# Kernel tuning notes

Measured on AMD Instinct MI355X. Metric: run time of the kernel, lower is better.

The kernel has to match this reference:

```python
import jax, jax.numpy as jnp
import numpy as np

KERNEL_SIZE = 9  # spatial kernel extent used only for output cropping


def setup_inputs() -> dict:
    key = jax.random.key(0)
    k1, k2, k3, k4 = jax.random.split(key, 4)
    B, Cin, Cout, H, W = 32, 64, 128, 128, 128
    Wf = W // 2 + 1  # rfft bins on last dim (W even, no pad branch)
    return {
        "signal": jax.random.normal(k1, (B, Cin, H, W), dtype=jnp.float32),
        "weight_real": jax.random.normal(k2, (Cout, Cin, H, Wf), dtype=jnp.float32),
        "weight_imag": jax.random.normal(k3, (Cout, Cin, H, Wf), dtype=jnp.float32),
        "bias": jax.random.normal(k4, (Cout,), dtype=jnp.float32),
    }


def reference(signal, weight_real, weight_imag, bias):
    # FFT conv with a frequency-domain complex kernel (groups=1, padding=0,
    # stride=1). Matches torch fft_conv: rfftn -> complex matmul over channels
    # per frequency bin -> irfftn -> crop -> bias add.
    B, Cin, H, W = signal.shape
    sig_fr = jnp.fft.rfftn(signal, axes=(2, 3))            # [B, Cin, H, W//2+1] c64
    kernel = (weight_real + 1j * weight_imag).astype(jnp.complex64)
    # complex_matmul with groups=1: contract Cin per (h,w) frequency bin
    out_fr = jnp.einsum('bihw,oihw->bohw', sig_fr, kernel)  # [B, Cout, H, W//2+1]
    out = jnp.fft.irfftn(out_fr, axes=(2, 3))               # [B, Cout, H, W] real
    Ho = H - KERNEL_SIZE + 1
    Wo = W - KERNEL_SIZE + 1
    out = out[:, :, :Ho, :Wo]
    out = out + bias[None, :, None, None]
    return out
```

## Files before the change

### kernel.cpp

```cpp
#include <hip/hip_runtime.h>
#include <math.h>

#define DI __device__ __forceinline__

constexpr int Hh   = 128;
constexpr int Ww   = 128;
constexpr int WF   = 65;
constexpr int NBIN = Hh * WF;
constexpr int NB   = 32;
constexpr int CIN  = 64;
constexpr int COUT = 128;
constexpr int HO   = 120;
constexpr int WO   = 120;

typedef __bf16 bf16x8 __attribute__((ext_vector_type(8)));
typedef float  f32x16 __attribute__((ext_vector_type(16)));

DI unsigned int bfbits(float x) {
  unsigned int u = __float_as_uint(x);
  return (u + 0x7FFFu + ((u >> 16) & 1u)) >> 16;
}
DI unsigned int packbf(float re, float im) { return bfbits(re) | (bfbits(im) << 16); }
DI float2 unpackbf(unsigned int v) {
  return make_float2(__uint_as_float(v << 16), __uint_as_float(v & 0xFFFF0000u));
}

DI f32x16 MFMA32(uint4 a, uint4 b, f32x16 c) {
  return __builtin_amdgcn_mfma_f32_32x32x16_bf16(
      __builtin_bit_cast(bf16x8, a), __builtin_bit_cast(bf16x8, b), c, 0, 0, 0);
}
DI unsigned int rotneg(unsigned int x) { return ((x << 16) | (x >> 16)) ^ 0x80000000u; }
DI uint4 derive(uint4 s) {
  uint4 r; r.x = rotneg(s.x); r.y = rotneg(s.y); r.z = rotneg(s.z); r.w = rotneg(s.w);
  return r;
}

DI void wsync() {
  asm volatile("s_waitcnt lgkmcnt(0)" ::: "memory");
  __builtin_amdgcn_sched_barrier(0);
}

DI float2* fft128x2(float2* s, float2* d, const float2* tw, int lane, int inv) {
  wsync();
#pragma unroll
  for (int st = 0; st < 7; ++st) {
    const int m  = 1 << st;
    const int tj = lane & ~(m - 1);
    float2 a0 = s[lane],       a1 = s[lane + 64];
    float2 b0 = s[lane + 128], b1 = s[lane + 192];
    float2 w  = tw[tj];
    const float wy = inv ? -w.y : w.y;
    const int di = lane + tj;
    {
      float sx = a0.x + a1.x, sy = a0.y + a1.y;
      float dx = a0.x - a1.x, dy = a0.y - a1.y;
      d[di]     = make_float2(sx, sy);
      d[di + m] = make_float2(w.x * dx - wy * dy, w.x * dy + wy * dx);
    }
    {
      float sx = b0.x + b1.x, sy = b0.y + b1.y;
      float dx = b0.x - b1.x, dy = b0.y - b1.y;
      d[di + 128]     = make_float2(sx, sy);
      d[di + 128 + m] = make_float2(w.x * dx - wy * dy, w.x * dy + wy * dx);
    }
    wsync();
    float2* t_ = s; s = d; d = t_;
  }
  return s;
}

__global__ __launch_bounds__(256) void fwd_fft(const float* __restrict__ sig,
                                               unsigned int* __restrict__ sf) {
  __shared__ unsigned int sImg[NBIN];
  __shared__ float2 bufA[4][256];
  __shared__ float2 bufB[4][256];
  __shared__ float2 tw[64];

  const int t = threadIdx.x, grp = t >> 6, lane = t & 63;
  const size_t img = blockIdx.x;
  const float* src = sig + img * (size_t)(Hh * Ww);
  unsigned int* dst = sf + img * (size_t)NBIN;

  if (t < 64) {
    float s_, c_;
    sincosf(-(float)M_PI * (float)t / 64.f, &s_, &c_);
    tw[t] = make_float2(c_, s_);
  }
  __syncthreads();

  for (int batch = 0; batch < 8; ++batch) {
#pragma unroll
    for (int f = 0; f < 2; ++f) {
      const int jp = batch * 8 + grp * 2 + f;
      const float* r0 = src + (size_t)(2 * jp) * Ww;
      bufA[grp][f * 128 + lane]      = make_float2(r0[lane],      r0[Ww + lane]);
      bufA[grp][f * 128 + 64 + lane] = make_float2(r0[lane + 64], r0[Ww + lane + 64]);
    }
    float2* Z = fft128x2(bufA[grp], bufB[grp], tw, lane, 0);
#pragma unroll
    for (int f = 0; f < 2; ++f) {
      const int jp = batch * 8 + grp * 2 + f;
      float2 Zk = Z[f * 128 + lane];
      float2 Zm = Z[f * 128 + ((128 - lane) & 127)];
      sImg[(2 * jp) * WF + lane]     = packbf(0.5f * (Zk.x + Zm.x), 0.5f * (Zk.y - Zm.y));
      sImg[(2 * jp + 1) * WF + lane] = packbf(0.5f * (Zk.y + Zm.y), 0.5f * (Zm.x - Zk.x));
      if (lane == 0) {
        float2 Z64 = Z[f * 128 + 64];
        sImg[(2 * jp) * WF + 64]     = packbf(Z64.x, 0.f);
        sImg[(2 * jp + 1) * WF + 64] = packbf(Z64.y, 0.f);
      }
    }
  }
  __syncthreads();

  for (int batch = 0; batch < 9; ++batch) {
#pragma unroll
    for (int f = 0; f < 2; ++f) {
      const int w  = batch * 8 + grp * 2 + f;
      const int wc = (w < WF) ? w : (WF - 1);
      bufA[grp][f * 128 + lane]      = unpackbf(sImg[lane * WF + wc]);
      bufA[grp][f * 128 + 64 + lane] = unpackbf(sImg[(lane + 64) * WF + wc]);
    }
    float2* R = fft128x2(bufA[grp], bufB[grp], tw, lane, 0);
#pragma unroll
    for (int f = 0; f < 2; ++f) {
      const int w = batch * 8 + grp * 2 + f;
      if (w < WF) {
        float2 a = R[f * 128 + lane], b = R[f * 128 + 64 + lane];
        sImg[lane * WF + w]        = packbf(a.x, a.y);
        sImg[(lane + 64) * WF + w] = packbf(b.x, b.y);
      }
    }
  }
  __syncthreads();

  const uint4* s4 = (const uint4*)sImg;
  uint4* d4 = (uint4*)dst;
  for (int idx = t; idx < NBIN / 4; idx += 256) d4[idx] = s4[idx];
}

constexpr int PT    = 16;
constexpr int PLANE = 260;

__global__ __launch_bounds__(512, 4) void spec_mm(const unsigned int* __restrict__ sf,
                                                  const float* __restrict__ wr,
                                                  const float* __restrict__ wi,
                                                  unsigned int* __restrict__ of) {
  __shared__ unsigned int wbuf[PT * PLANE];
  __shared__ unsigned int sbuf[PT * PLANE];

  const int t = threadIdx.x;
  const int bid = blockIdx.x;
  const int swz = (bid & 7) * 260 + (bid >> 3);
  const int o0 = (swz & 3) * 32;
  const int p0 = (swz >> 2) * PT;

  const int po = t & 3;
  const int ii = (t >> 2) & 7;
  const int rl = (t >> 5) & 15;

  const float* wrp0 = wr + ((size_t)(o0 + rl) * CIN + ii) * NBIN + p0 + po * 4;
  const float* wip0 = wi + ((size_t)(o0 + rl) * CIN + ii) * NBIN + p0 + po * 4;
  const unsigned int* sfp0 = sf + ((size_t)rl * CIN + ii) * NBIN + p0 + po * 4;
  const size_t rowAdv = (size_t)16 * CIN * NBIN;

  auto slotOf = [](int row, int i) {
    return ((((row * 2) + (i >> 2)) ^ ((row >> 2) & 7)) << 2) + (i & 3);
  };
  const int slotLo = slotOf(rl, ii);
  const int slotHi = slotOf(rl + 16, ii);

  const int l = t & 63, wv = t >> 6;
  const int lr = l & 31, lq = l >> 5;
  const int moff = ((((lr * 2) + lq) ^ ((lr >> 2) & 7)) << 2);
  const int pA = 2 * wv, pB = 2 * wv + 1;

  f32x16 aR0 = {}, aI0 = {}, aR1 = {}, aI1 = {};

  float4 w0r, w1r, w0i, w1i; uint4 s0v, s1v;
  {
    w0r = *(const float4*)(wrp0);          w1r = *(const float4*)(wrp0 + rowAdv);
    w0i = *(const float4*)(wip0);          w1i = *(const float4*)(wip0 + rowAdv);
    s0v = *(const uint4*)(sfp0);           s1v = *(const uint4*)(sfp0 + rowAdv);
  }

  for (int kq = 0; kq < 8; ++kq) {
    const float* a0 = (const float*)&w0r;  const float* a1 = (const float*)&w1r;
    const float* b0 = (const float*)&w0i;  const float* b1 = (const float*)&w1i;
    const unsigned int* u0 = (const unsigned int*)&s0v;
    const unsigned int* u1 = (const unsigned int*)&s1v;
#pragma unroll
    for (int j = 0; j < 4; ++j) {
      const int pp = (po * 4 + j) * PLANE;
      wbuf[pp + slotLo] = packbf(a0[j], -b0[j]);
      wbuf[pp + slotHi] = packbf(a1[j], -b1[j]);
      sbuf[pp + slotLo] = u0[j];
      sbuf[pp + slotHi] = u1[j];
    }
    if (kq < 7) {
      const size_t adv = (size_t)(kq + 1) * 8 * NBIN;
      w0r = *(const float4*)(wrp0 + adv);          w1r = *(const float4*)(wrp0 + adv + rowAdv);
      w0i = *(const float4*)(wip0 + adv);          w1i = *(const float4*)(wip0 + adv + rowAdv);
      s0v = *(const uint4*)(sfp0 + adv);           s1v = *(const uint4*)(sfp0 + adv + rowAdv);
    }
    __syncthreads();

    {
      const uint4 a  = *(const uint4*)&wbuf[pA * PLANE + moff];
      const uint4 s  = *(const uint4*)&sbuf[pA * PLANE + moff];
      aR0 = MFMA32(a, s, aR0);
      aI0 = MFMA32(a, derive(s), aI0);
    }
    {
      const uint4 a  = *(const uint4*)&wbuf[pB * PLANE + moff];
      const uint4 s  = *(const uint4*)&sbuf[pB * PLANE + moff];
      aR1 = MFMA32(a, s, aR1);
      aI1 = MFMA32(a, derive(s), aI1);
    }
    __syncthreads();
  }

  const int b = lr;
#pragma unroll
  for (int r = 0; r < 16; ++r) {
    const int o = o0 + (r & 3) + 8 * (r >> 2) + 4 * lq;
    uint2 v;
    v.x = packbf(aR0[r], aI0[r]);
    v.y = packbf(aR1[r], aI1[r]);
    *(uint2*)(of + ((size_t)b * COUT + o) * NBIN + p0 + 2 * wv) = v;
  }
}

__global__ __launch_bounds__(256) void inv_fft(const unsigned int* __restrict__ of,
                                               const float* __restrict__ bias,
                                               float* __restrict__ out) {
  __shared__ unsigned int sImg[NBIN];
  __shared__ float2 bufA[4][256];
  __shared__ float2 bufB[4][256];
  __shared__ float2 tw[64];

  const int t = threadIdx.x, grp = t >> 6, lane = t & 63;
  const size_t img = blockIdx.x;
  const unsigned int* src = of + img * (size_t)NBIN;
  float* dst = out + img * (size_t)(HO * WO);
  const float bo = bias[img & (COUT - 1)];

  if (t < 64) {
    float s_, c_;
    sincosf(-(float)M_PI * (float)t / 64.f, &s_, &c_);
    tw[t] = make_float2(c_, s_);
  }

  const uint4* s4 = (const uint4*)src;
  uint4* d4 = (uint4*)sImg;
  for (int idx = t; idx < NBIN / 4; idx += 256) d4[idx] = s4[idx];
  __syncthreads();

  for (int batch = 0; batch < 9; ++batch) {
#pragma unroll
    for (int f = 0; f < 2; ++f) {
      const int w  = batch * 8 + grp * 2 + f;
      const int wc = (w < WF) ? w : (WF - 1);
      bufA[grp][f * 128 + lane]      = unpackbf(sImg[lane * WF + wc]);
      bufA[grp][f * 128 + 64 + lane] = unpackbf(sImg[(lane + 64) * WF + wc]);
    }
    float2* R = fft128x2(bufA[grp], bufB[grp], tw, lane, 1);
#pragma unroll
    for (int f = 0; f < 2; ++f) {
      const int w = batch * 8 + grp * 2 + f;
      if (w < WF) {
        float2 a = R[f * 128 + lane], b = R[f * 128 + 64 + lane];
        sImg[lane * WF + w]        = packbf(a.x, a.y);
        sImg[(lane + 64) * WF + w] = packbf(b.x, b.y);
      }
    }
  }
  __syncthreads();

  const float scale = 1.f / 16384.f;
  for (int batch = 0; batch < 8; ++batch) {
#pragma unroll
    for (int f = 0; f < 2; ++f) {
      const int jp = batch * 8 + grp * 2 + f;
      const int jc = (jp < 60) ? jp : 59;
      const unsigned int* X0p = &sImg[(size_t)(2 * jc) * WF];
      const unsigned int* X1p = X0p + WF;
      float2 za, zb;
      if (lane == 0) {
        za = make_float2(unpackbf(X0p[0]).x,  unpackbf(X1p[0]).x);
        zb = make_float2(unpackbf(X0p[64]).x, unpackbf(X1p[64]).x);
      } else {
        float2 x0 = unpackbf(X0p[lane]), x1 = unpackbf(X1p[lane]);
        za = make_float2(x0.x - x1.y, x0.y + x1.x);
        const int mI = 64 - lane;
        float2 y0 = unpackbf(X0p[mI]), y1 = unpackbf(X1p[mI]);
        zb = make_float2(y0.x + y1.y, y1.x - y0.y);
      }
      bufA[grp][f * 128 + lane]      = za;
      bufA[grp][f * 128 + 64 + lane] = zb;
    }
    float2* R = fft128x2(bufA[grp], bufB[grp], tw, lane, 1);
#pragma unroll
    for (int f = 0; f < 2; ++f) {
      const int jp = batch * 8 + grp * 2 + f;
      if (jp < 60) {
        float2 v0 = R[f * 128 + lane];
        dst[(size_t)(2 * jp) * WO + lane]     = v0.x * scale + bo;
        dst[(size_t)(2 * jp + 1) * WO + lane] = v0.y * scale + bo;
        if (lane < WO - 64) {
          float2 v1 = R[f * 128 + 64 + lane];
          dst[(size_t)(2 * jp) * WO + lane + 64]     = v1.x * scale + bo;
          dst[(size_t)(2 * jp + 1) * WO + lane + 64] = v1.y * scale + bo;
        }
      }
    }
  }
}

extern "C" void kernel_launch(void* const* d_in, const int* in_sizes, int n_in,
                              void* d_out, int out_size, void* d_ws, size_t ws_size,
                              hipStream_t stream) {
  const float* signal = (const float*)d_in[0];
  const float* wr     = (const float*)d_in[1];
  const float* wi     = (const float*)d_in[2];
  const float* bias   = (const float*)d_in[3];
  float* out = (float*)d_out;

  unsigned int* sig_fr = (unsigned int*)d_out;
  unsigned int* out_fr = (unsigned int*)d_ws;
  (void)in_sizes; (void)n_in; (void)out_size; (void)ws_size;

  fwd_fft<<<NB * CIN, 256, 0, stream>>>(signal, sig_fr);
  spec_mm<<<2080, 512, 0, stream>>>(sig_fr, wr, wi, out_fr);
  inv_fft<<<NB * COUT, 256, 0, stream>>>(out_fr, bias, out);
}
```

Before: 546.7 us.

## Use wave-shuffle register FFTs and double-buffer spec_mm global prefetch

```diff
diff --git a/kernel.cpp b/kernel.cpp
--- a/kernel.cpp
+++ b/kernel.cpp
@@ -40,95 +40,121 @@
   __builtin_amdgcn_sched_barrier(0);
 }
 
-DI float2* fft128x2(float2* s, float2* d, const float2* tw, int lane, int inv) {
-  wsync();
-#pragma unroll
-  for (int st = 0; st < 7; ++st) {
-    const int m  = 1 << st;
-    const int tj = lane & ~(m - 1);
-    float2 a0 = s[lane],       a1 = s[lane + 64];
-    float2 b0 = s[lane + 128], b1 = s[lane + 192];
-    float2 w  = tw[tj];
-    const float wy = inv ? -w.y : w.y;
-    const int di = lane + tj;
-    {
-      float sx = a0.x + a1.x, sy = a0.y + a1.y;
-      float dx = a0.x - a1.x, dy = a0.y - a1.y;
-      d[di]     = make_float2(sx, sy);
-      d[di + m] = make_float2(w.x * dx - wy * dy, w.x * dy + wy * dx);
-    }
-    {
-      float sx = b0.x + b1.x, sy = b0.y + b1.y;
-      float dx = b0.x - b1.x, dy = b0.y - b1.y;
-      d[di + 128]     = make_float2(sx, sy);
-      d[di + 128 + m] = make_float2(w.x * dx - wy * dy, w.x * dy + wy * dx);
-    }
-    wsync();
-    float2* t_ = s; s = d; d = t_;
-  }
-  return s;
+DI int bitrev6(int l) {
+  return ((l & 1) << 5) | ((l & 2) << 3) | ((l & 4) << 1) |
+         ((l & 8) >> 1) | ((l & 16) >> 3) | ((l & 32) >> 5);
+}
+DI float2 cmul(float2 a, float2 b) {
+  return make_float2(a.x * b.x - a.y * b.y, a.x * b.y + a.y * b.x);
+}
+DI float2 sxor(float2 v, int m) {
+  return make_float2(__shfl_xor(v.x, m), __shfl_xor(v.y, m));
+}
+DI void stg(float2& v, int h, float2 tw, int l) {
+  float2 p = sxor(v, h);
+  float2 s = make_float2(v.x + p.x, v.y + p.y);
+  float2 d = make_float2(p.x - v.x, p.y - v.y);
+  float2 m = cmul(d, tw);
+  v = (l & h) ? m : s;
+}
+DI void stg1(float2& v, int l) {
+  float2 p = sxor(v, 1);
+  v = (l & 1) ? make_float2(p.x - v.x, p.y - v.y)
+              : make_float2(v.x + p.x, v.y + p.y);
+}
+DI void twinit(float2* tw, int l) {
+  float s_, c_;
+  sincosf(-(float)M_PI * (float)l / 64.f, &s_, &c_);
+  tw[0] = make_float2(c_, s_);
+#pragma unroll
+  for (int i = 0; i < 5; ++i) {
+    const int h = 32 >> i;
+    sincosf(-(float)M_PI * (float)(l & (h - 1)) / (float)h, &s_, &c_);
+    tw[1 + i] = make_float2(c_, s_);
+  }
+}
+DI void sfft128x2(float2& a0, float2& b0, float2& a1, float2& b1,
+                  const float2* tw, int l) {
+  {
+    float2 s = make_float2(a0.x + b0.x, a0.y + b0.y);
+    float2 d = make_float2(a0.x - b0.x, a0.y - b0.y);
+    a0 = s; b0 = cmul(d, tw[0]);
+  }
+  {
+    float2 s = make_float2(a1.x + b1.x, a1.y + b1.y);
+    float2 d = make_float2(a1.x - b1.x, a1.y - b1.y);
+    a1 = s; b1 = cmul(d, tw[0]);
+  }
+#pragma unroll
+  for (int i = 0; i < 5; ++i) {
+    const int h = 32 >> i;
+    stg(a0, h, tw[1 + i], l); stg(a1, h, tw[1 + i], l);
+    stg(b0, h, tw[1 + i], l); stg(b1, h, tw[1 + i], l);
+  }
+  stg1(a0, l); stg1(a1, l); stg1(b0, l); stg1(b1, l);
 }
 
 __global__ __launch_bounds__(256) void fwd_fft(const float* __restrict__ sig,
                                                unsigned int* __restrict__ sf) {
   __shared__ unsigned int sImg[NBIN];
-  __shared__ float2 bufA[4][256];
-  __shared__ float2 bufB[4][256];
-  __shared__ float2 tw[64];
-
-  const int t = threadIdx.x, grp = t >> 6, lane = t & 63;
+  __shared__ __align__(16) float2 rowbuf[4][2][128];
+
+  const int t = threadIdx.x, grp = t >> 6, l = t & 63;
   const size_t img = blockIdx.x;
   const float* src = sig + img * (size_t)(Hh * Ww);
   unsigned int* dst = sf + img * (size_t)NBIN;
 
-  if (t < 64) {
-    float s_, c_;
-    sincosf(-(float)M_PI * (float)t / 64.f, &s_, &c_);
-    tw[t] = make_float2(c_, s_);
-  }
-  __syncthreads();
+  float2 tw[6]; twinit(tw, l);
+  const int br = bitrev6(l);
 
   for (int batch = 0; batch < 8; ++batch) {
+    float2 a[2], b[2];
 #pragma unroll
     for (int f = 0; f < 2; ++f) {
       const int jp = batch * 8 + grp * 2 + f;
       const float* r0 = src + (size_t)(2 * jp) * Ww;
-      bufA[grp][f * 128 + lane]      = make_float2(r0[lane],      r0[Ww + lane]);
-      bufA[grp][f * 128 + 64 + lane] = make_float2(r0[lane + 64], r0[Ww + lane + 64]);
-    }
-    float2* Z = fft128x2(bufA[grp], bufB[grp], tw, lane, 0);
+      a[f] = make_float2(r0[l],      r0[Ww + l]);
+      b[f] = make_float2(r0[64 + l], r0[Ww + 64 + l]);
+    }
+    sfft128x2(a[0], b[0], a[1], b[1], tw, l);
+#pragma unroll
+    for (int f = 0; f < 2; ++f) {
+      *(float4*)&rowbuf[grp][f][2 * br] =
+          make_float4(a[f].x, a[f].y, b[f].x, b[f].y);
+    }
+    wsync();
 #pragma unroll
     for (int f = 0; f < 2; ++f) {
       const int jp = batch * 8 + grp * 2 + f;
-      float2 Zk = Z[f * 128 + lane];
-      float2 Zm = Z[f * 128 + ((128 - lane) & 127)];
-      sImg[(2 * jp) * WF + lane]     = packbf(0.5f * (Zk.x + Zm.x), 0.5f * (Zk.y - Zm.y));
-      sImg[(2 * jp + 1) * WF + lane] = packbf(0.5f * (Zk.y + Zm.y), 0.5f * (Zm.x - Zk.x));
-      if (lane == 0) {
-        float2 Z64 = Z[f * 128 + 64];
+      float2 Zk = rowbuf[grp][f][l];
+      float2 Zm = rowbuf[grp][f][(128 - l) & 127];
+      sImg[(2 * jp) * WF + l]     = packbf(0.5f * (Zk.x + Zm.x), 0.5f * (Zk.y - Zm.y));
+      sImg[(2 * jp + 1) * WF + l] = packbf(0.5f * (Zk.y + Zm.y), 0.5f * (Zm.x - Zk.x));
+      if (l == 0) {
+        float2 Z64 = rowbuf[grp][f][64];
         sImg[(2 * jp) * WF + 64]     = packbf(Z64.x, 0.f);
         sImg[(2 * jp + 1) * WF + 64] = packbf(Z64.y, 0.f);
       }
     }
+    wsync();
   }
   __syncthreads();
 
   for (int batch = 0; batch < 9; ++batch) {
-#pragma unroll
-    for (int f = 0; f < 2; ++f) {
-      const int w  = batch * 8 + grp * 2 + f;
+    float2 a[2], b[2]; int wcol[2];
+#pragma unroll
+    for (int f = 0; f < 2; ++f) {
+      const int w = batch * 8 + grp * 2 + f; wcol[f] = w;
       const int wc = (w < WF) ? w : (WF - 1);
-      bufA[grp][f * 128 + lane]      = unpackbf(sImg[lane * WF + wc]);
-      bufA[grp][f * 128 + 64 + lane] = unpackbf(sImg[(lane + 64) * WF + wc]);
-    }
-    float2* R = fft128x2(bufA[grp], bufB[grp], tw, lane, 0);
-#pragma unroll
-    for (int f = 0; f < 2; ++f) {
-      const int w = batch * 8 + grp * 2 + f;
-      if (w < WF) {
-        float2 a = R[f * 128 + lane], b = R[f * 128 + 64 + lane];
-        sImg[lane * WF + w]        = packbf(a.x, a.y);
-        sImg[(lane + 64) * WF + w] = packbf(b.x, b.y);
+      a[f] = unpackbf(sImg[l * WF + wc]);
+      b[f] = unpackbf(sImg[(l + 64) * WF + wc]);
+    }
+    sfft128x2(a[0], b[0], a[1], b[1], tw, l);
+#pragma unroll
+    for (int f = 0; f < 2; ++f) {
+      if (wcol[f] < WF) {
+        sImg[(2 * br) * WF + wcol[f]]     = packbf(a[f].x, a[f].y);
+        sImg[(2 * br + 1) * WF + wcol[f]] = packbf(b[f].x, b[f].y);
       }
     }
   }
@@ -142,7 +168,7 @@
 constexpr int PT    = 16;
 constexpr int PLANE = 260;
 
-__global__ __launch_bounds__(512, 4) void spec_mm(const unsigned int* __restrict__ sf,
+__global__ __launch_bounds__(512, 3) void spec_mm(const unsigned int* __restrict__ sf,
                                                   const float* __restrict__ wr,
                                                   const float* __restrict__ wi,
                                                   unsigned int* __restrict__ of) {
@@ -177,43 +203,50 @@
 
   f32x16 aR0 = {}, aI0 = {}, aR1 = {}, aI1 = {};
 
-  float4 w0r, w1r, w0i, w1i; uint4 s0v, s1v;
-  {
-    w0r = *(const float4*)(wrp0);          w1r = *(const float4*)(wrp0 + rowAdv);
-    w0i = *(const float4*)(wip0);          w1i = *(const float4*)(wip0 + rowAdv);
-    s0v = *(const uint4*)(sfp0);           s1v = *(const uint4*)(sfp0 + rowAdv);
-  }
-
+  float4 w0r[2], w1r[2], w0i[2], w1i[2]; uint4 s0v[2], s1v[2];
+
+#pragma unroll
+  for (int s = 0; s < 2; ++s) {
+    const size_t adv = (size_t)s * 8 * NBIN;
+    w0r[s] = *(const float4*)(wrp0 + adv);  w1r[s] = *(const float4*)(wrp0 + adv + rowAdv);
+    w0i[s] = *(const float4*)(wip0 + adv);  w1i[s] = *(const float4*)(wip0 + adv + rowAdv);
+    s0v[s] = *(const uint4*)(sfp0 + adv);   s1v[s] = *(const uint4*)(sfp0 + adv + rowAdv);
+  }
+
+#pragma unroll
   for (int kq = 0; kq < 8; ++kq) {
-    const float* a0 = (const float*)&w0r;  const float* a1 = (const float*)&w1r;
-    const float* b0 = (const float*)&w0i;  const float* b1 = (const float*)&w1i;
-    const unsigned int* u0 = (const unsigned int*)&s0v;
-    const unsigned int* u1 = (const unsigned int*)&s1v;
-#pragma unroll
-    for (int j = 0; j < 4; ++j) {
-      const int pp = (po * 4 + j) * PLANE;
-      wbuf[pp + slotLo] = packbf(a0[j], -b0[j]);
-      wbuf[pp + slotHi] = packbf(a1[j], -b1[j]);
-      sbuf[pp + slotLo] = u0[j];
-      sbuf[pp + slotHi] = u1[j];
-    }
-    if (kq < 7) {
-      const size_t adv = (size_t)(kq + 1) * 8 * NBIN;
-      w0r = *(const float4*)(wrp0 + adv);          w1r = *(const float4*)(wrp0 + adv + rowAdv);
-      w0i = *(const float4*)(wip0 + adv);          w1i = *(const float4*)(wip0 + adv + rowAdv);
-      s0v = *(const uint4*)(sfp0 + adv);           s1v = *(const uint4*)(sfp0 + adv + rowAdv);
+    const int cs = kq & 1;
+    {
+      const float* a0 = (const float*)&w0r[cs]; const float* a1 = (const float*)&w1r[cs];
+      const float* b0 = (const float*)&w0i[cs]; const float* b1 = (const float*)&w1i[cs];
+      const unsigned int* u0 = (const unsigned int*)&s0v[cs];
+      const unsigned int* u1 = (const unsigned int*)&s1v[cs];
+#pragma unroll
+      for (int j = 0; j < 4; ++j) {
+        const int pp = (po * 4 + j) * PLANE;
+        wbuf[pp + slotLo] = packbf(a0[j], -b0[j]);
+        wbuf[pp + slotHi] = packbf(a1[j], -b1[j]);
+        sbuf[pp + slotLo] = u0[j];
+        sbuf[pp + slotHi] = u1[j];
+      }
+    }
+    if (kq < 6) {
+      const size_t adv = (size_t)(kq + 2) * 8 * NBIN;
+      w0r[cs] = *(const float4*)(wrp0 + adv);  w1r[cs] = *(const float4*)(wrp0 + adv + rowAdv);
+      w0i[cs] = *(const float4*)(wip0 + adv);  w1i[cs] = *(const float4*)(wip0 + adv + rowAdv);
+      s0v[cs] = *(const uint4*)(sfp0 + adv);   s1v[cs] = *(const uint4*)(sfp0 + adv + rowAdv);
     }
     __syncthreads();
 
     {
-      const uint4 a  = *(const uint4*)&wbuf[pA * PLANE + moff];
-      const uint4 s  = *(const uint4*)&sbuf[pA * PLANE + moff];
+      const uint4 a = *(const uint4*)&wbuf[pA * PLANE + moff];
+      const uint4 s = *(const uint4*)&sbuf[pA * PLANE + moff];
       aR0 = MFMA32(a, s, aR0);
       aI0 = MFMA32(a, derive(s), aI0);
     }
     {
-      const uint4 a  = *(const uint4*)&wbuf[pB * PLANE + moff];
-      const uint4 s  = *(const uint4*)&sbuf[pB * PLANE + moff];
+      const uint4 a = *(const uint4*)&wbuf[pB * PLANE + moff];
+      const uint4 s = *(const uint4*)&sbuf[pB * PLANE + moff];
       aR1 = MFMA32(a, s, aR1);
       aI1 = MFMA32(a, derive(s), aI1);
     }
@@ -235,21 +268,15 @@
                                                const float* __restrict__ bias,
                                                float* __restrict__ out) {
   __shared__ unsigned int sImg[NBIN];
-  __shared__ float2 bufA[4][256];
-  __shared__ float2 bufB[4][256];
-  __shared__ float2 tw[64];
-
-  const int t = threadIdx.x, grp = t >> 6, lane = t & 63;
+
+  const int t = threadIdx.x, grp = t >> 6, l = t & 63;
   const size_t img = blockIdx.x;
   const unsigned int* src = of + img * (size_t)NBIN;
   float* dst = out + img * (size_t)(HO * WO);
   const float bo = bias[img & (COUT - 1)];
 
-  if (t < 64) {
-    float s_, c_;
-    sincosf(-(float)M_PI * (float)t / 64.f, &s_, &c_);
-    tw[t] = make_float2(c_, s_);
-  }
+  float2 tw[6]; twinit(tw, l);
+  const int br = bitrev6(l);
 
   const uint4* s4 = (const uint4*)src;
   uint4* d4 = (uint4*)sImg;
@@ -257,61 +284,60 @@
   __syncthreads();
 
   for (int batch = 0; batch < 9; ++batch) {
-#pragma unroll
-    for (int f = 0; f < 2; ++f) {
-      const int w  = batch * 8 + grp * 2 + f;
+    float2 a[2], b[2]; int wcol[2];
+#pragma unroll
+    for (int f = 0; f < 2; ++f) {
+      const int w = batch * 8 + grp * 2 + f; wcol[f] = w;
       const int wc = (w < WF) ? w : (WF - 1);
-      bufA[grp][f * 128 + lane]      = unpackbf(sImg[lane * WF + wc]);
-      bufA[grp][f * 128 + 64 + lane] = unpackbf(sImg[(lane + 64) * WF + wc]);
-    }
-    float2* R = fft128x2(bufA[grp], bufB[grp], tw, lane, 1);
-#pragma unroll
-    for (int f = 0; f < 2; ++f) {
-      const int w = batch * 8 + grp * 2 + f;
-      if (w < WF) {
-        float2 a = R[f * 128 + lane], b = R[f * 128 + 64 + lane];
-        sImg[lane * WF + w]        = packbf(a.x, a.y);
-        sImg[(lane + 64) * WF + w] = packbf(b.x, b.y);
+      float2 za = unpackbf(sImg[l * WF + wc]);
+      float2 zb = unpackbf(sImg[(l + 64) * WF + wc]);
+      a[f] = make_float2(za.x, -za.y);
+      b[f] = make_float2(zb.x, -zb.y);
+    }
+    sfft128x2(a[0], b[0], a[1], b[1], tw, l);
+#pragma unroll
+    for (int f = 0; f < 2; ++f) {
+      if (wcol[f] < WF) {
+        sImg[(2 * br) * WF + wcol[f]]     = packbf(a[f].x, -a[f].y);
+        sImg[(2 * br + 1) * WF + wcol[f]] = packbf(b[f].x, -b[f].y);
       }
     }
   }
   __syncthreads();
 
-  const float scale = 1.f / 16384.f;
+  const float sc = 1.f / 16384.f;
   for (int batch = 0; batch < 8; ++batch) {
-#pragma unroll
-    for (int f = 0; f < 2; ++f) {
-      const int jp = batch * 8 + grp * 2 + f;
+    float2 a[2], b[2]; int jpv[2];
+#pragma unroll
+    for (int f = 0; f < 2; ++f) {
+      const int jp = batch * 8 + grp * 2 + f; jpv[f] = jp;
       const int jc = (jp < 60) ? jp : 59;
       const unsigned int* X0p = &sImg[(size_t)(2 * jc) * WF];
       const unsigned int* X1p = X0p + WF;
       float2 za, zb;
-      if (lane == 0) {
+      if (l == 0) {
         za = make_float2(unpackbf(X0p[0]).x,  unpackbf(X1p[0]).x);
         zb = make_float2(unpackbf(X0p[64]).x, unpackbf(X1p[64]).x);
       } else {
-        float2 x0 = unpackbf(X0p[lane]), x1 = unpackbf(X1p[lane]);
+        float2 x0 = unpackbf(X0p[l]), x1 = unpackbf(X1p[l]);
         za = make_float2(x0.x - x1.y, x0.y + x1.x);
-        const int mI = 64 - lane;
+        const int mI = 64 - l;
         float2 y0 = unpackbf(X0p[mI]), y1 = unpackbf(X1p[mI]);
         zb = make_float2(y0.x + y1.y, y1.x - y0.y);
       }
-      bufA[grp][f * 128 + lane]      = za;
-      bufA[grp][f * 128 + 64 + lane] = zb;
-    }
-    float2* R = fft128x2(bufA[grp], bufB[grp], tw, lane, 1);
-#pragma unroll
-    for (int f = 0; f < 2; ++f) {
-      const int jp = batch * 8 + grp * 2 + f;
-      if (jp < 60) {
-        float2 v0 = R[f * 128 + lane];
-        dst[(size_t)(2 * jp) * WO + lane]     = v0.x * scale + bo;
-        dst[(size_t)(2 * jp + 1) * WO + lane] = v0.y * scale + bo;
-        if (lane < WO - 64) {
-          float2 v1 = R[f * 128 + 64 + lane];
-          dst[(size_t)(2 * jp) * WO + lane + 64]     = v1.x * scale + bo;
-          dst[(size_t)(2 * jp + 1) * WO + lane + 64] = v1.y * scale + bo;
-        }
+      a[f] = make_float2(za.x, -za.y);
+      b[f] = make_float2(zb.x, -zb.y);
+    }
+    sfft128x2(a[0], b[0], a[1], b[1], tw, l);
+    const int n0 = 2 * br;
+#pragma unroll
+    for (int f = 0; f < 2; ++f) {
+      const int jp = jpv[f];
+      if (jp < 60 && n0 < WO) {
+        float2 r0 = make_float2(a[f].x * sc + bo,  b[f].x * sc + bo);
+        float2 r1 = make_float2(-a[f].y * sc + bo, -b[f].y * sc + bo);
+        *(float2*)(dst + (size_t)(2 * jp) * WO + n0)     = r0;
+        *(float2*)(dst + (size_t)(2 * jp + 1) * WO + n0) = r1;
       }
     }
   }
```

After: 517.0 us. 5.4% less time.
